# Kernel tuning notes

Hardware: AMD Instinct MI355X
Metric: run time of the kernel (lower is better)

## Reference

```python
import jax, jax.numpy as jnp
import numpy as np

KERN = 2  # matches init kwarg


def _avgpool(x):
    # non-overlapping avg pool kernel=stride=KERN on (N,C,H,W)
    N, C, H, W = x.shape
    return x.reshape(N, C, H // KERN, KERN, W // KERN, KERN).mean(axis=(3, 5))


def _pair_sum(mu1, var1, mu2, var2):
    # mu*, var*: (N, D). Broadcast to (N, N, D) and reduce to scalar.
    d = mu1[:, None, :] - mu2[None, :, :]
    s = var1[:, None, :] + var2[None, :, :]
    return jnp.sum(jnp.exp(-0.5 * (d * d / s + jnp.log(s))))


def setup_inputs() -> dict:
    key = jax.random.key(0)
    k1, k2, k3, k4 = jax.random.split(key, 4)
    shp = (128, 16, 32, 32)
    return {
        "mu_a": jax.random.normal(k1, shp, dtype=jnp.float32),
        "logvar_a": jax.random.normal(k2, shp, dtype=jnp.float32),
        "mu_b": jax.random.normal(k3, shp, dtype=jnp.float32),
        "logvar_b": jax.random.normal(k4, shp, dtype=jnp.float32),
    }


def reference(mu_a, logvar_a, mu_b, logvar_b):
    inv_k2 = 1.0 / (KERN * KERN)
    ma = _avgpool(mu_a)
    mb = _avgpool(mu_b)
    va = _avgpool(jnp.exp(logvar_a)) * inv_k2
    vb = _avgpool(jnp.exp(logvar_b)) * inv_k2
    N = ma.shape[0]
    ma, mb = ma.reshape(N, -1), mb.reshape(N, -1)
    va, vb = va.reshape(N, -1), vb.reshape(N, -1)
    vaa = _pair_sum(ma, va, ma, va)
    vab = _pair_sum(ma, va, mb, vb)
    vbb = _pair_sum(mb, vb, mb, vb)
    return vaa + vbb - 2.0 * vab
```

## Files before the change

kernel.cpp:

```cpp
#include <hip/hip_runtime.h>

#define NN 128
#define CC_ 16
#define HH 32
#define WW 32
#define DD 4096
#define ND (NN*DD)

typedef float v2f __attribute__((ext_vector_type(2)));

#define MU_SCALE 0.8493218002880191f

__global__ __launch_bounds__(256) void pool_kernel(
    const float* __restrict__ mu_a, const float* __restrict__ lv_a,
    const float* __restrict__ mu_b, const float* __restrict__ lv_b,
    float2* __restrict__ wm, float2* __restrict__ wv, float* __restrict__ out)
{
    int t = blockIdx.x * 256 + threadIdx.x;
    if (t == 0) out[0] = 0.0f;

    int wo = t & 15;
    int ho = (t >> 4) & 15;
    int c  = (t >> 8) & 15;
    int n  = t >> 12;

    int base = ((n * CC_ + c) * HH + 2 * ho) * WW + 2 * wo;

    float2 a0 = *(const float2*)(mu_a + base);
    float2 a1 = *(const float2*)(mu_a + base + WW);
    float2 la0 = *(const float2*)(lv_a + base);
    float2 la1 = *(const float2*)(lv_a + base + WW);
    float2 b0 = *(const float2*)(mu_b + base);
    float2 b1 = *(const float2*)(mu_b + base + WW);
    float2 lb0 = *(const float2*)(lv_b + base);
    float2 lb1 = *(const float2*)(lv_b + base + WW);

    const float ms = 0.25f * MU_SCALE;
    float ma_v = ms * (a0.x + a0.y + a1.x + a1.y);
    float mb_v = ms * (b0.x + b0.y + b1.x + b1.y);
    float va_v = 0.0625f * (__expf(la0.x) + __expf(la0.y) + __expf(la1.x) + __expf(la1.y));
    float vb_v = 0.0625f * (__expf(lb0.x) + __expf(lb0.y) + __expf(lb1.x) + __expf(lb1.y));

    wm[t] = make_float2(ma_v, mb_v);
    wv[t] = make_float2(va_v, vb_v);
}

__device__ __forceinline__ void pair_group(
    v2f& acc, v2f mi, v2f mj, v2f vi, v2f vj)
{
    v2f dd = mi - mj;
    v2f s  = vi + vj;
    v2f r;
    r.x = __builtin_amdgcn_rsqf(s.x);
    r.y = __builtin_amdgcn_rsqf(s.y);
    v2f q  = dd * r;
    v2f qq = q * q;
    v2f e;
    e.x = __builtin_amdgcn_exp2f(-qq.x);
    e.y = __builtin_amdgcn_exp2f(-qq.y);
    acc += e * r;
}

__device__ __forceinline__ void pair_group_w(
    v2f& acc, float w, v2f mi, v2f mj, v2f vi, v2f vj)
{
    v2f dd = mi - mj;
    v2f s  = vi + vj;
    v2f r;
    r.x = __builtin_amdgcn_rsqf(s.x);
    r.y = __builtin_amdgcn_rsqf(s.y);
    v2f q  = dd * r;
    v2f qq = q * q;
    v2f e;
    e.x = __builtin_amdgcn_exp2f(-qq.x);
    e.y = __builtin_amdgcn_exp2f(-qq.y);
    v2f er = e * r;
    acc += (v2f){w, w} * er;
}

__global__ __launch_bounds__(256, 4) void pair_kernel(
    const float2* __restrict__ wm, const float2* __restrict__ wv,
    float* __restrict__ out)
{
    const int d = blockIdx.x * 256 + threadIdx.x;
    const int y = blockIdx.y;

    float part;

    if (y < 136) {
        int ti = (int)((sqrtf(8.0f * (float)y + 1.0f) - 1.0f) * 0.5f + 1e-4f);
        int tj = y - ti * (ti + 1) / 2;
        const int i0 = ti * 8, j0 = tj * 8;

        v2f pm[8], pv[8];
#pragma unroll
        for (int p = 0; p < 8; ++p) {
            float2 m = wm[(i0 + p) * DD + d];
            float2 v = wv[(i0 + p) * DD + d];
            pm[p] = (v2f){m.x, m.y};
            pv[p] = (v2f){v.x, v.y};
        }

        v2f acc0 = (v2f){0.0f, 0.0f};
        v2f acc1 = (v2f){0.0f, 0.0f};
        if (ti != tj) {
#pragma unroll 2
            for (int jj = 0; jj < 8; ++jj) {
                float2 mjf = wm[(j0 + jj) * DD + d];
                float2 vjf = wv[(j0 + jj) * DD + d];
                v2f mj = (v2f){mjf.x, mjf.y};
                v2f vj = (v2f){vjf.x, vjf.y};
#pragma unroll
                for (int p = 0; p < 4; ++p)
                    pair_group(acc0, pm[p], mj, pv[p], vj);
#pragma unroll
                for (int p = 4; p < 8; ++p)
                    pair_group(acc1, pm[p], mj, pv[p], vj);
            }
        } else {
#pragma unroll 2
            for (int jj = 0; jj < 8; ++jj) {
                float2 mjf = wm[(j0 + jj) * DD + d];
                float2 vjf = wv[(j0 + jj) * DD + d];
                v2f mj = (v2f){mjf.x, mjf.y};
                v2f vj = (v2f){vjf.x, vjf.y};
                int j = j0 + jj;
#pragma unroll
                for (int p = 0; p < 4; ++p) {
                    int i = i0 + p;
                    float w = (j < i) ? 1.0f : ((j == i) ? 0.5f : 0.0f);
                    pair_group_w(acc0, w, pm[p], mj, pv[p], vj);
                }
#pragma unroll
                for (int p = 4; p < 8; ++p) {
                    int i = i0 + p;
                    float w = (j < i) ? 1.0f : ((j == i) ? 0.5f : 0.0f);
                    pair_group_w(acc1, w, pm[p], mj, pv[p], vj);
                }
            }
        }
        v2f acc = acc0 + acc1;
        part = 2.0f * (acc.x + acc.y);
    } else {
        const int y2 = y - 136;
        const int i0 = (y2 >> 2) * 4;
        const int j0 = (y2 & 3) * 32;

        v2f pma[2], pva[2];
#pragma unroll
        for (int p = 0; p < 2; ++p) {
            float2 m0 = wm[(i0 + 2 * p) * DD + d];
            float2 m1 = wm[(i0 + 2 * p + 1) * DD + d];
            float2 v0 = wv[(i0 + 2 * p) * DD + d];
            float2 v1 = wv[(i0 + 2 * p + 1) * DD + d];
            pma[p] = (v2f){m0.x, m1.x};
            pva[p] = (v2f){v0.x, v1.x};
        }

        v2f acc0 = (v2f){0.0f, 0.0f};
        v2f acc1 = (v2f){0.0f, 0.0f};
#pragma unroll 2
        for (int j = j0; j < j0 + 32; ++j) {
            float2 jm = wm[j * DD + d];
            float2 jv = wv[j * DD + d];
            v2f jmb2 = (v2f){jm.y, jm.y};
            v2f jvb2 = (v2f){jv.y, jv.y};
            pair_group(acc0, pma[0], jmb2, pva[0], jvb2);
            pair_group(acc1, pma[1], jmb2, pva[1], jvb2);
        }
        v2f acc = acc0 + acc1;
        part = -2.0f * (acc.x + acc.y);
    }

#pragma unroll
    for (int off = 32; off > 0; off >>= 1)
        part += __shfl_down(part, off, 64);

    __shared__ float wsum[4];
    int lane = threadIdx.x & 63;
    int wv_  = threadIdx.x >> 6;
    if (lane == 0) wsum[wv_] = part;
    __syncthreads();
    if (threadIdx.x == 0) {
        float s = wsum[0] + wsum[1] + wsum[2] + wsum[3];
        atomicAdd(out, s);
    }
}

extern "C" void kernel_launch(void* const* d_in, const int* in_sizes, int n_in,
                              void* d_out, int out_size, void* d_ws, size_t ws_size,
                              hipStream_t stream) {
    const float* mu_a = (const float*)d_in[0];
    const float* lv_a = (const float*)d_in[1];
    const float* mu_b = (const float*)d_in[2];
    const float* lv_b = (const float*)d_in[3];
    float* out = (float*)d_out;
    float2* wm = (float2*)d_ws;
    float2* wv = ((float2*)d_ws) + ND;

    pool_kernel<<<dim3(ND / 256), 256, 0, stream>>>(mu_a, lv_a, mu_b, lv_b, wm, wv, out);
    pair_kernel<<<dim3(DD / 256, 136 + 128), 256, 0, stream>>>(wm, wv, out);
}
```

Measured before the change: 139.9 us.

## Retile pair kernel with 4x16 triangular tiles and 8x16 cross tiles

Changes the self-pair triangular tiling from 8x8 tiles over 136 blocks to 4x16 row-by-column tiles over 144 blocks, with a new index decode. The cross-pair section now uses 8 rows by 16 columns per block instead of 4 by 32. This keeps fewer rows in registers in the self-pair path and more in the cross path, and removes the occupancy hint from launch bounds. Intent is to balance register pressure, occupancy and reuse of each loaded j element. The trade-off is slightly more wasted work on diagonal tiles and a different reuse ratio.

```diff
diff --git a/kernel.cpp b/kernel.cpp
--- a/kernel.cpp
+++ b/kernel.cpp
@@ -78,7 +78,7 @@
     acc += (v2f){w, w} * er;
 }
 
-__global__ __launch_bounds__(256, 4) void pair_kernel(
+__global__ __launch_bounds__(256) void pair_kernel(
     const float2* __restrict__ wm, const float2* __restrict__ wv,
     float* __restrict__ out)
 {
@@ -87,14 +87,19 @@
 
     float part;
 
-    if (y < 136) {
-        int ti = (int)((sqrtf(8.0f * (float)y + 1.0f) - 1.0f) * 0.5f + 1e-4f);
-        int tj = y - ti * (ti + 1) / 2;
-        const int i0 = ti * 8, j0 = tj * 8;
-
-        v2f pm[8], pv[8];
-#pragma unroll
-        for (int p = 0; p < 8; ++p) {
+    if (y < 144) {
+        int g = (int)((sqrtf(2.0f * (float)y + 1.0f) - 1.0f) * 0.5f);
+        while (2 * (g + 1) * (g + 2) <= y) ++g;
+        while (2 * g * (g + 1) > y) --g;
+        int rem = y - 2 * g * (g + 1);
+        int ti = 4 * g + rem / (g + 1);
+        int tj = rem % (g + 1);
+        const int i0 = ti * 4, j0 = tj * 16;
+        const bool has_diag = (tj == (ti >> 2));
+
+        v2f pm[4], pv[4];
+#pragma unroll
+        for (int p = 0; p < 4; ++p) {
             float2 m = wm[(i0 + p) * DD + d];
             float2 v = wv[(i0 + p) * DD + d];
             pm[p] = (v2f){m.x, m.y};
@@ -103,23 +108,21 @@
 
         v2f acc0 = (v2f){0.0f, 0.0f};
         v2f acc1 = (v2f){0.0f, 0.0f};
-        if (ti != tj) {
-#pragma unroll 2
-            for (int jj = 0; jj < 8; ++jj) {
+        if (!has_diag) {
+#pragma unroll 4
+            for (int jj = 0; jj < 16; ++jj) {
                 float2 mjf = wm[(j0 + jj) * DD + d];
                 float2 vjf = wv[(j0 + jj) * DD + d];
                 v2f mj = (v2f){mjf.x, mjf.y};
                 v2f vj = (v2f){vjf.x, vjf.y};
-#pragma unroll
-                for (int p = 0; p < 4; ++p)
-                    pair_group(acc0, pm[p], mj, pv[p], vj);
-#pragma unroll
-                for (int p = 4; p < 8; ++p)
-                    pair_group(acc1, pm[p], mj, pv[p], vj);
+                pair_group(acc0, pm[0], mj, pv[0], vj);
+                pair_group(acc1, pm[1], mj, pv[1], vj);
+                pair_group(acc0, pm[2], mj, pv[2], vj);
+                pair_group(acc1, pm[3], mj, pv[3], vj);
             }
         } else {
-#pragma unroll 2
-            for (int jj = 0; jj < 8; ++jj) {
+#pragma unroll 4
+            for (int jj = 0; jj < 16; ++jj) {
                 float2 mjf = wm[(j0 + jj) * DD + d];
                 float2 vjf = wv[(j0 + jj) * DD + d];
                 v2f mj = (v2f){mjf.x, mjf.y};
@@ -129,26 +132,20 @@
                 for (int p = 0; p < 4; ++p) {
                     int i = i0 + p;
                     float w = (j < i) ? 1.0f : ((j == i) ? 0.5f : 0.0f);
-                    pair_group_w(acc0, w, pm[p], mj, pv[p], vj);
-                }
-#pragma unroll
-                for (int p = 4; p < 8; ++p) {
-                    int i = i0 + p;
-                    float w = (j < i) ? 1.0f : ((j == i) ? 0.5f : 0.0f);
-                    pair_group_w(acc1, w, pm[p], mj, pv[p], vj);
+                    pair_group_w((p & 1) ? acc1 : acc0, w, pm[p], mj, pv[p], vj);
                 }
             }
         }
         v2f acc = acc0 + acc1;
         part = 2.0f * (acc.x + acc.y);
     } else {
-        const int y2 = y - 136;
-        const int i0 = (y2 >> 2) * 4;
-        const int j0 = (y2 & 3) * 32;
-
-        v2f pma[2], pva[2];
-#pragma unroll
-        for (int p = 0; p < 2; ++p) {
+        const int y2 = y - 144;
+        const int i0 = (y2 >> 3) * 8;
+        const int j0 = (y2 & 7) * 16;
+
+        v2f pma[4], pva[4];
+#pragma unroll
+        for (int p = 0; p < 4; ++p) {
             float2 m0 = wm[(i0 + 2 * p) * DD + d];
             float2 m1 = wm[(i0 + 2 * p + 1) * DD + d];
             float2 v0 = wv[(i0 + 2 * p) * DD + d];
@@ -159,14 +156,16 @@
 
         v2f acc0 = (v2f){0.0f, 0.0f};
         v2f acc1 = (v2f){0.0f, 0.0f};
-#pragma unroll 2
-        for (int j = j0; j < j0 + 32; ++j) {
-            float2 jm = wm[j * DD + d];
-            float2 jv = wv[j * DD + d];
+#pragma unroll 4
+        for (int jj = 0; jj < 16; ++jj) {
+            float2 jm = wm[(j0 + jj) * DD + d];
+            float2 jv = wv[(j0 + jj) * DD + d];
             v2f jmb2 = (v2f){jm.y, jm.y};
             v2f jvb2 = (v2f){jv.y, jv.y};
             pair_group(acc0, pma[0], jmb2, pva[0], jvb2);
             pair_group(acc1, pma[1], jmb2, pva[1], jvb2);
+            pair_group(acc0, pma[2], jmb2, pva[2], jvb2);
+            pair_group(acc1, pma[3], jmb2, pva[3], jvb2);
         }
         v2f acc = acc0 + acc1;
         part = -2.0f * (acc.x + acc.y);
@@ -199,5 +198,5 @@
     float2* wv = ((float2*)d_ws) + ND;
 
     pool_kernel<<<dim3(ND / 256), 256, 0, stream>>>(mu_a, lv_a, mu_b, lv_b, wm, wv, out);
-    pair_kernel<<<dim3(DD / 256, 136 + 128), 256, 0, stream>>>(wm, wv, out);
-}
+    pair_kernel<<<dim3(DD / 256, 144 + 128), 256, 0, stream>>>(wm, wv, out);
+}
```

After: 140.6 us. No clear change (+0.5%).
